# Kernel tuning notes

Hardware: AMD Instinct MI355X
Metric: run time of the kernel (lower is better)

The kernel has to match this reference:

```python
import jax, jax.numpy as jnp
import numpy as np

N_NODES = 50000
N_EDGES = 500000
N_REL = 50


def _linear(x, w, b):
    return x @ w.T + b


def _sage(x, src, dst, w_l, b_l, w_r, n_nodes):
    # PyG SAGEConv (mean aggr): out = lin_l(mean_{j in N(i)} x_j) + lin_r(x_i)
    msg = x[src]                                            # [E, F]
    s = jax.ops.segment_sum(msg, dst, num_segments=n_nodes)  # [N, F]
    cnt = jax.ops.segment_sum(jnp.ones((src.shape[0],), x.dtype), dst, num_segments=n_nodes)
    mean = s / jnp.clip(cnt, 1.0)[:, None]
    return mean @ w_l.T + b_l + x @ w_r.T


def setup_inputs() -> dict:
    key = jax.random.key(0)
    ks = jax.random.split(key, 24)

    def g(k, shape, fan_in):
        return jax.random.normal(k, shape, dtype=jnp.float32) * (1.0 / np.sqrt(fan_in))

    x = jax.random.normal(ks[0], (N_NODES, 16), dtype=jnp.float32)
    edge_index = jax.random.randint(ks[1], (2, N_EDGES), 0, N_NODES, dtype=jnp.int32)
    y = jax.random.randint(ks[2], (N_EDGES,), 0, N_REL, dtype=jnp.int32)

    return {
        "x": x, "edge_index": edge_index, "y": y,
        # SAGEConv 1: 16 -> 64
        "w1_l": g(ks[3], (64, 16), 16), "b1": jnp.zeros((64,), jnp.float32), "w1_r": g(ks[4], (64, 16), 16),
        # SAGEConv 2: 64 -> 128
        "w2_l": g(ks[5], (128, 64), 64), "b2": jnp.zeros((128,), jnp.float32), "w2_r": g(ks[6], (128, 64), 64),
        # object_fc: 256->128->64->32->16
        "of_w1": g(ks[7], (128, 256), 256), "of_b1": jnp.zeros((128,), jnp.float32),
        "of_w2": g(ks[8], (64, 128), 128), "of_b2": jnp.zeros((64,), jnp.float32),
        "of_w3": g(ks[9], (32, 64), 64), "of_b3": jnp.zeros((32,), jnp.float32),
        "of_w4": g(ks[10], (16, 32), 32), "of_b4": jnp.zeros((16,), jnp.float32),
        # relation_fc: 16->8->4->N_REL
        "rf_w1": g(ks[11], (8, 16), 16), "rf_b1": jnp.zeros((8,), jnp.float32),
        "rf_w2": g(ks[12], (4, 8), 8), "rf_b2": jnp.zeros((4,), jnp.float32),
        "rf_w3": g(ks[13], (N_REL, 4), 4), "rf_b3": jnp.zeros((N_REL,), jnp.float32),
    }


def reference(x, edge_index, y,
              w1_l, b1, w1_r, w2_l, b2, w2_r,
              of_w1, of_b1, of_w2, of_b2, of_w3, of_b3, of_w4, of_b4,
              rf_w1, rf_b1, rf_w2, rf_b2, rf_w3, rf_b3):
    src, dst = edge_index[0], edge_index[1]
    n = x.shape[0]

    h = jax.nn.relu(_sage(x, src, dst, w1_l, b1, w1_r, n))      # [N, 64]
    h = jax.nn.relu(_sage(h, src, dst, w2_l, b2, w2_r, n))      # [N, 128]

    # Batched version of the per-edge loop: gather endpoints, concat, MLP.
    feat = jnp.concatenate([h[src], h[dst]], axis=-1)           # [E, 256]
    o = jax.nn.relu(_linear(feat, of_w1, of_b1))   # dropout = identity (eval)
    o = jax.nn.relu(_linear(o, of_w2, of_b2))
    o = jax.nn.relu(_linear(o, of_w3, of_b3))
    o = _linear(o, of_w4, of_b4)                                # [E, 16]

    r = jax.nn.relu(_linear(o, rf_w1, rf_b1))
    r = jax.nn.relu(_linear(r, rf_w2, rf_b2))
    r = _linear(r, rf_w3, rf_b3)                                # [E, N_REL]
    return r, y
```

## Files before the change

### kernel.cpp

```cpp
#include <hip/hip_runtime.h>
#include <hip/hip_bf16.h>

#define N_NODES 50000
#define N_EDGES 500000
#define N_REL   50
#define NTILES  ((N_EDGES + 63) / 64)
#define PBLOCKS 512
#define NODE_TILES ((N_NODES + 63) / 64)

#define CNT_OFF 0
#define S1_OFF  (N_NODES)
#define S2_OFF  (S1_OFF + N_NODES*16)
#define ZERO_FLOATS (S2_OFF + N_NODES*64)
#define H1_OFF  ZERO_FLOATS
#define H2_OFF  (H1_OFF + N_NODES*64)

typedef short short8  __attribute__((ext_vector_type(8)));
typedef short short4v __attribute__((ext_vector_type(4)));
typedef float f32x4   __attribute__((ext_vector_type(4)));
typedef float f4      __attribute__((ext_vector_type(4)));

#define MFMA16(a,b,c) __builtin_amdgcn_mfma_f32_16x16x32_bf16((a),(b),(c),0,0,0)

__device__ __forceinline__ short f2bf(float x) {
    unsigned u = __float_as_uint(x);
    unsigned r = (u + 0x7fffu + ((u >> 16) & 1u)) >> 16;
    return (short)r;
}

__device__ __forceinline__ short8 load_wfrag(const float* __restrict__ W, int row, int K, int k) {
    const f4* p = (const f4*)(W + (size_t)row * K + k);
    f4 a = p[0], b = p[1];
    short8 r;
    r[0] = f2bf(a[0]); r[1] = f2bf(a[1]); r[2] = f2bf(a[2]); r[3] = f2bf(a[3]);
    r[4] = f2bf(b[0]); r[5] = f2bf(b[1]); r[6] = f2bf(b[2]); r[7] = f2bf(b[3]);
    return r;
}


__global__ __launch_bounds__(256) void k_scatter1(
    const float* __restrict__ x, const int* __restrict__ src,
    const int* __restrict__ dst, float* __restrict__ s1, float* __restrict__ cnt)
{
    int t = blockIdx.x * blockDim.x + threadIdx.x;
    if (t >= N_EDGES * 16) return;
    int e = t >> 4, f = t & 15;
    int s = src[e], d = dst[e];
    atomicAdd(&s1[d * 16 + f], x[s * 16 + f]);
    if (f == 0) atomicAdd(&cnt[d], 1.0f);
}

__global__ __launch_bounds__(256) void k_scatter2(
    const float* __restrict__ h1, const int* __restrict__ src,
    const int* __restrict__ dst, float* __restrict__ s2)
{
    long long t = (long long)blockIdx.x * blockDim.x + threadIdx.x;
    if (t >= (long long)N_EDGES * 64) return;
    int e = (int)(t >> 6), f = (int)(t & 63);
    atomicAdd(&s2[(long long)dst[e] * 64 + f], h1[(long long)src[e] * 64 + f]);
}

__global__ __launch_bounds__(256) void k_sage1_mfma(
    const float* __restrict__ x, const float* __restrict__ s1,
    const float* __restrict__ cnt,
    const float* __restrict__ w1_l, const float* __restrict__ b1,
    const float* __restrict__ w1_r, float* __restrict__ h1)
{
    __shared__ short feat[64 * 40];

    const int t    = threadIdx.x;
    const int w    = t >> 6;
    const int lane = t & 63;
    const int lr   = lane & 15;
    const int lg   = lane >> 4;
    const int base = blockIdx.x * 64;

    short8 w1f;
    if (lg < 2) w1f = load_wfrag(w1_l, w * 16 + lr, 16, lg * 8);
    else        w1f = load_wfrag(w1_r, w * 16 + lr, 16, (lg - 2) * 8);

    {
        int e  = t >> 2, q = t & 3;
        int ng = base + e;
        short8 v = (short8)0;
        if (ng < N_NODES) {
            if (q < 2) {
                float c = cnt[ng];
                c = c < 1.0f ? 1.0f : c;
                float inv = 1.0f / c;
                f4 a = *(const f4*)(s1 + (size_t)ng * 16 + q * 8);
                f4 b = *(const f4*)(s1 + (size_t)ng * 16 + q * 8 + 4);
#pragma unroll
                for (int j = 0; j < 4; ++j) { v[j] = f2bf(a[j] * inv); v[4 + j] = f2bf(b[j] * inv); }
            } else {
                f4 a = *(const f4*)(x + (size_t)ng * 16 + (q - 2) * 8);
                f4 b = *(const f4*)(x + (size_t)ng * 16 + (q - 2) * 8 + 4);
#pragma unroll
                for (int j = 0; j < 4; ++j) { v[j] = f2bf(a[j]); v[4 + j] = f2bf(b[j]); }
            }
        }
        *(short8*)&feat[e * 40 + q * 8] = v;
    }
    __syncthreads();

    f32x4 acc[4];
    f4 bia = *(const f4*)&b1[w * 16 + lg * 4];
#pragma unroll
    for (int nt = 0; nt < 4; ++nt) {
        acc[nt][0] = bia[0]; acc[nt][1] = bia[1]; acc[nt][2] = bia[2]; acc[nt][3] = bia[3];
    }
#pragma unroll
    for (int nt = 0; nt < 4; ++nt) {
        int e = nt * 16 + lr;
        short8 bf = *(const short8*)&feat[e * 40 + lg * 8];
        acc[nt] = MFMA16(w1f, bf, acc[nt]);
    }
#pragma unroll
    for (int nt = 0; nt < 4; ++nt) {
        int ng = base + nt * 16 + lr;
        if (ng < N_NODES) {
            f4 o;
#pragma unroll
            for (int r = 0; r < 4; ++r) { float v = acc[nt][r]; o[r] = v > 0.0f ? v : 0.0f; }
            *(f4*)&h1[(size_t)ng * 64 + w * 16 + lg * 4] = o;
        }
    }
}

__global__ __launch_bounds__(256) void k_sage2_mfma(
    const float* __restrict__ h1, const float* __restrict__ s2,
    const float* __restrict__ cnt,
    const float* __restrict__ w2_l, const float* __restrict__ b2,
    const float* __restrict__ w2_r, float* __restrict__ h2)
{
    __shared__ short feat[64 * 128];

    const int t    = threadIdx.x;
    const int w    = t >> 6;
    const int lane = t & 63;
    const int lr   = lane & 15;
    const int lg   = lane >> 4;
    const int base = blockIdx.x * 64;

    short8 wf[2][4];
#pragma unroll
    for (int mt = 0; mt < 2; ++mt)
#pragma unroll
        for (int kt = 0; kt < 4; ++kt) {
            int row = w * 32 + mt * 16 + lr;
            int k   = kt * 32 + lg * 8;
            wf[mt][kt] = (k < 64) ? load_wfrag(w2_r, row, 64, k)
                                  : load_wfrag(w2_l, row, 64, k - 64);
        }

    {
        int e  = t >> 2, q = t & 3;
        int ng = base + e;
        float inv = 1.0f;
        const float* srcp = nullptr;
        if (ng < N_NODES) {
            if (q < 2) {
                srcp = h1 + (size_t)ng * 64 + q * 32;
            } else {
                float c = cnt[ng];
                c = c < 1.0f ? 1.0f : c;
                inv = 1.0f / c;
                srcp = s2 + (size_t)ng * 64 + (q - 2) * 32;
            }
        }
#pragma unroll
        for (int j = 0; j < 4; ++j) {
            short8 v = (short8)0;
            if (srcp) {
                f4 a = *(const f4*)(srcp + j * 8);
                f4 b = *(const f4*)(srcp + j * 8 + 4);
#pragma unroll
                for (int q2 = 0; q2 < 4; ++q2) { v[q2] = f2bf(a[q2] * inv); v[4 + q2] = f2bf(b[q2] * inv); }
            }
            int cc   = q * 4 + j;
            int scol = (cc * 8) ^ ((e & 7) << 3);
            *(short8*)&feat[e * 128 + scol] = v;
        }
    }
    __syncthreads();

    f32x4 acc[2][4];
#pragma unroll
    for (int mt = 0; mt < 2; ++mt) {
        f4 bia = *(const f4*)&b2[w * 32 + mt * 16 + lg * 4];
#pragma unroll
        for (int nt = 0; nt < 4; ++nt) {
            acc[mt][nt][0] = bia[0]; acc[mt][nt][1] = bia[1];
            acc[mt][nt][2] = bia[2]; acc[mt][nt][3] = bia[3];
        }
    }
#pragma unroll
    for (int kt = 0; kt < 4; ++kt) {
        short8 bf[4];
#pragma unroll
        for (int nt = 0; nt < 4; ++nt) {
            int e = nt * 16 + lr;
            int k = kt * 32 + lg * 8;
            int scol = k ^ ((e & 7) << 3);
            bf[nt] = *(const short8*)&feat[e * 128 + scol];
        }
#pragma unroll
        for (int mt = 0; mt < 2; ++mt)
#pragma unroll
            for (int nt = 0; nt < 4; ++nt)
                acc[mt][nt] = MFMA16(wf[mt][kt], bf[nt], acc[mt][nt]);
    }
#pragma unroll
    for (int mt = 0; mt < 2; ++mt)
#pragma unroll
        for (int nt = 0; nt < 4; ++nt) {
            int ng = base + nt * 16 + lr;
            if (ng < N_NODES) {
                f4 o;
#pragma unroll
                for (int r = 0; r < 4; ++r) { float v = acc[mt][nt][r]; o[r] = v > 0.0f ? v : 0.0f; }
                *(f4*)&h2[(size_t)ng * 128 + w * 32 + mt * 16 + lg * 4] = o;
            }
        }
}

__global__ __launch_bounds__(256, 2) void k_edge_fused(
    const float* __restrict__ h2, const int* __restrict__ src,
    const int* __restrict__ dst, const int* __restrict__ y,
    const float* __restrict__ ow1, const float* __restrict__ ob1,
    const float* __restrict__ ow2, const float* __restrict__ ob2,
    const float* __restrict__ ow3, const float* __restrict__ ob3,
    const float* __restrict__ ow4, const float* __restrict__ ob4,
    const float* __restrict__ rw1, const float* __restrict__ rb1,
    const float* __restrict__ rw2, const float* __restrict__ rb2,
    const float* __restrict__ rw3, const float* __restrict__ rb3,
    float* __restrict__ out)
{
    __shared__ short feat[64 * 256];
    __shared__ short act1[64 * 128];
    __shared__ float act4[64 * 17];
    __shared__ float act6[64 * 4];
    __shared__ float sw[662];

    short* act2 = feat;
    short* act3 = feat + 64 * 64;

    const int t    = threadIdx.x;
    const int w    = t >> 6;
    const int lane = t & 63;
    const int lr   = lane & 15;
    const int lg   = lane >> 4;

    if (t < 128) sw[t]       = ob1[t];
    if (t < 64)  sw[128 + t] = ob2[t];
    if (t < 32)  sw[192 + t] = ob3[t];
    if (t < 16)  sw[224 + t] = ob4[t];
    if (t < 8)   sw[240 + t] = rb1[t];
    if (t < 4)   sw[248 + t] = rb2[t];
    if (t < 50)  sw[252 + t] = rb3[t];
    if (t < 128) sw[302 + t] = rw1[t];
    if (t < 32)  sw[430 + t] = rw2[t];
    if (t < 200) sw[462 + t] = rw3[t];

    short8 w1f[2][8];
#pragma unroll
    for (int mt = 0; mt < 2; ++mt)
#pragma unroll
        for (int kt = 0; kt < 8; ++kt)
            w1f[mt][kt] = load_wfrag(ow1, w * 32 + mt * 16 + lr, 256, kt * 32 + lg * 8);

    short8 w2f[4];
#pragma unroll
    for (int kt = 0; kt < 4; ++kt)
        w2f[kt] = load_wfrag(ow2, w * 16 + lr, 128, kt * 32 + lg * 8);

    short8 w3f[2][2];
#pragma unroll
    for (int mt = 0; mt < 2; ++mt)
#pragma unroll
        for (int kt = 0; kt < 2; ++kt)
            w3f[mt][kt] = load_wfrag(ow3, mt * 16 + lr, 64, kt * 32 + lg * 8);

    short8 w4f = load_wfrag(ow4, lr, 32, lg * 8);

    for (int tile = blockIdx.x; tile < NTILES; tile += PBLOCKS) {
        const int base = tile * 64;

        {
            int e    = t >> 2;
            int half = (t >> 1) & 1;
            int eg   = base + e;
            const float* np = nullptr;
            if (eg < N_EDGES) {
                int node = half ? dst[eg] : src[eg];
                np = h2 + (size_t)node * 128 + (t & 1) * 64;
            }
#pragma unroll
            for (int j = 0; j < 8; ++j) {
                short8 v;
                if (np) {
                    f4 a = *(const f4*)(np + j * 8);
                    f4 b = *(const f4*)(np + j * 8 + 4);
                    v[0] = f2bf(a[0]); v[1] = f2bf(a[1]); v[2] = f2bf(a[2]); v[3] = f2bf(a[3]);
                    v[4] = f2bf(b[0]); v[5] = f2bf(b[1]); v[6] = f2bf(b[2]); v[7] = f2bf(b[3]);
                } else {
                    v = (short8)0;
                }
                int cc   = half * 16 + (t & 1) * 8 + j;
                int scol = (cc * 8) ^ ((e & 7) << 3);
                *(short8*)&feat[e * 256 + scol] = v;
            }
        }
        __syncthreads();

        {
            f32x4 acc[2][4];
#pragma unroll
            for (int mt = 0; mt < 2; ++mt) {
                f32x4 bia;
#pragma unroll
                for (int r = 0; r < 4; ++r) bia[r] = sw[w * 32 + mt * 16 + lg * 4 + r];
#pragma unroll
                for (int nt = 0; nt < 4; ++nt) acc[mt][nt] = bia;
            }
#pragma unroll
            for (int kt = 0; kt < 8; ++kt) {
                short8 bf[4];
#pragma unroll
                for (int nt = 0; nt < 4; ++nt) {
                    int e = nt * 16 + lr;
                    int k = kt * 32 + lg * 8;
                    int scol = k ^ ((e & 7) << 3);
                    bf[nt] = *(const short8*)&feat[e * 256 + scol];
                }
#pragma unroll
                for (int mt = 0; mt < 2; ++mt)
#pragma unroll
                    for (int nt = 0; nt < 4; ++nt)
                        acc[mt][nt] = MFMA16(w1f[mt][kt], bf[nt], acc[mt][nt]);
            }
#pragma unroll
            for (int mt = 0; mt < 2; ++mt)
#pragma unroll
                for (int nt = 0; nt < 4; ++nt) {
                    int e  = nt * 16 + lr;
                    int n0 = w * 32 + mt * 16 + lg * 4;
                    short4v s;
#pragma unroll
                    for (int r = 0; r < 4; ++r) {
                        float v = acc[mt][nt][r];
                        s[r] = f2bf(v > 0.0f ? v : 0.0f);
                    }
                    int scol = n0 ^ ((e & 7) << 3);
                    *(short4v*)&act1[e * 128 + scol] = s;
                }
        }
        __syncthreads();

        {
            f32x4 acc[4];
            f32x4 bia;
#pragma unroll
            for (int r = 0; r < 4; ++r) bia[r] = sw[128 + w * 16 + lg * 4 + r];
#pragma unroll
            for (int nt = 0; nt < 4; ++nt) acc[nt] = bia;
#pragma unroll
            for (int kt = 0; kt < 4; ++kt) {
#pragma unroll
                for (int nt = 0; nt < 4; ++nt) {
                    int e = nt * 16 + lr;
                    int k = kt * 32 + lg * 8;
                    int scol = k ^ ((e & 7) << 3);
                    short8 bf = *(const short8*)&act1[e * 128 + scol];
                    acc[nt] = MFMA16(w2f[kt], bf, acc[nt]);
                }
            }
#pragma unroll
            for (int nt = 0; nt < 4; ++nt) {
                int e  = nt * 16 + lr;
                int n0 = w * 16 + lg * 4;
                short4v s;
#pragma unroll
                for (int r = 0; r < 4; ++r) {
                    float v = acc[nt][r];
                    s[r] = f2bf(v > 0.0f ? v : 0.0f);
                }
                int scol = n0 ^ ((e & 7) << 3);
                *(short4v*)&act2[e * 64 + scol] = s;
            }
        }
        __syncthreads();

        {
            const int e3 = w * 16 + lr;
            f32x4 acc[2];
#pragma unroll
            for (int mt = 0; mt < 2; ++mt) {
#pragma unroll
                for (int r = 0; r < 4; ++r) acc[mt][r] = sw[192 + mt * 16 + lg * 4 + r];
            }
#pragma unroll
            for (int kt = 0; kt < 2; ++kt) {
                int k = kt * 32 + lg * 8;
                int scol = k ^ ((e3 & 7) << 3);
                short8 bf = *(const short8*)&act2[e3 * 64 + scol];
#pragma unroll
                for (int mt = 0; mt < 2; ++mt)
                    acc[mt] = MFMA16(w3f[mt][kt], bf, acc[mt]);
            }
#pragma unroll
            for (int mt = 0; mt < 2; ++mt) {
                short4v s;
#pragma unroll
                for (int r = 0; r < 4; ++r) {
                    float v = acc[mt][r];
                    s[r] = f2bf(v > 0.0f ? v : 0.0f);
                }
                *(short4v*)&act3[e3 * 32 + mt * 16 + lg * 4] = s;
            }

            short8 bf = *(const short8*)&act3[e3 * 32 + lg * 8];
            f32x4 a4;
#pragma unroll
            for (int r = 0; r < 4; ++r) a4[r] = sw[224 + lg * 4 + r];
            a4 = MFMA16(w4f, bf, a4);
#pragma unroll
            for (int r = 0; r < 4; ++r) act4[e3 * 17 + lg * 4 + r] = a4[r];
        }
        __syncthreads();

        if (t < 64) {
            float a16[16];
#pragma unroll
            for (int f = 0; f < 16; ++f) a16[f] = act4[t * 17 + f];
            float a8[8];
#pragma unroll
            for (int o = 0; o < 8; ++o) {
                float v = sw[240 + o];
#pragma unroll
                for (int f = 0; f < 16; ++f) v += a16[f] * sw[302 + o * 16 + f];
                a8[o] = v > 0.0f ? v : 0.0f;
            }
            float a4v[4];
#pragma unroll
            for (int o = 0; o < 4; ++o) {
                float v = sw[248 + o];
#pragma unroll
                for (int f = 0; f < 8; ++f) v += a8[f] * sw[430 + o * 8 + f];
                a4v[o] = v > 0.0f ? v : 0.0f;
            }
#pragma unroll
            for (int q = 0; q < 4; ++q) act6[t * 4 + q] = a4v[q];
            int eg = base + t;
            if (eg < N_EDGES) out[(size_t)N_EDGES * N_REL + eg] = (float)y[eg];
        }
        __syncthreads();

#pragma unroll
        for (int i = 0; i < 13; ++i) {
            int idx = t + i * 256;
            if (idx < 64 * N_REL) {
                int e  = idx / N_REL;
                int r  = idx - e * N_REL;
                int eg = base + e;
                if (eg < N_EDGES) {
                    float v = sw[252 + r];
#pragma unroll
                    for (int f = 0; f < 4; ++f) v += act6[e * 4 + f] * sw[462 + r * 4 + f];
                    out[(size_t)base * N_REL + idx] = v;
                }
            }
        }
        __syncthreads();
    }
}

extern "C" void kernel_launch(void* const* d_in, const int* in_sizes, int n_in,
                              void* d_out, int out_size, void* d_ws, size_t ws_size,
                              hipStream_t stream) {
    const float* x    = (const float*)d_in[0];
    const int*   ei   = (const int*)d_in[1];
    const int*   src  = ei;
    const int*   dst  = ei + N_EDGES;
    const int*   y    = (const int*)d_in[2];
    const float* w1_l = (const float*)d_in[3];
    const float* b1   = (const float*)d_in[4];
    const float* w1_r = (const float*)d_in[5];
    const float* w2_l = (const float*)d_in[6];
    const float* b2   = (const float*)d_in[7];
    const float* w2_r = (const float*)d_in[8];
    const float* ow1  = (const float*)d_in[9];
    const float* ob1  = (const float*)d_in[10];
    const float* ow2  = (const float*)d_in[11];
    const float* ob2  = (const float*)d_in[12];
    const float* ow3  = (const float*)d_in[13];
    const float* ob3  = (const float*)d_in[14];
    const float* ow4  = (const float*)d_in[15];
    const float* ob4  = (const float*)d_in[16];
    const float* rw1  = (const float*)d_in[17];
    const float* rb1  = (const float*)d_in[18];
    const float* rw2  = (const float*)d_in[19];
    const float* rb2  = (const float*)d_in[20];
    const float* rw3  = (const float*)d_in[21];
    const float* rb3  = (const float*)d_in[22];

    float* ws  = (float*)d_ws;
    float* cnt = ws + CNT_OFF;
    float* s1  = ws + S1_OFF;
    float* s2  = ws + S2_OFF;
    float* h1  = ws + H1_OFF;
    float* h2  = ws + H2_OFF;
    float* out = (float*)d_out;

    hipMemsetAsync(d_ws, 0, (size_t)ZERO_FLOATS * sizeof(float), stream);

    {
        int total = N_EDGES * 16;
        k_scatter1<<<(total + 255) / 256, 256, 0, stream>>>(x, src, dst, s1, cnt);
    }
    k_sage1_mfma<<<NODE_TILES, 256, 0, stream>>>(x, s1, cnt, w1_l, b1, w1_r, h1);
    {
        long long total = (long long)N_EDGES * 64;
        k_scatter2<<<(int)((total + 255) / 256), 256, 0, stream>>>(h1, src, dst, s2);
    }
    k_sage2_mfma<<<NODE_TILES, 256, 0, stream>>>(h1, s2, cnt, w2_l, b2, w2_r, h2);

    k_edge_fused<<<PBLOCKS, 256, 0, stream>>>(
        h2, src, dst, y,
        ow1, ob1, ow2, ob2, ow3, ob3, ow4, ob4,
        rw1, rb1, rw2, rb2, rw3, rb3, out);
}
```

Measured before the change: 479.8 us.

## Store hidden activations in bf16, DMA edge gathers to LDS, per-wave MLP tail

Writes h1 and h2 as bf16 instead of fp32, which halves the gather traffic in the second scatter and the edge kernel. The edge kernel now gathers endpoint features directly into LDS with global_load_lds in a swizzled layout. The small relation MLP tail becomes a per-wave computation using wave barriers instead of block-wide syncs, and its scratch reuses the act1 buffer. Grid size and the occupancy hint rise from 2 to 3 blocks per CU. The bf16 rounding of h1 before aggregation adds a small precision loss.

After: 806.8 us. +68.2%, slower.

```diff
diff --git a/kernel.cpp b/kernel.cpp
--- a/kernel.cpp
+++ b/kernel.cpp
@@ -5,7 +5,7 @@
 #define N_EDGES 500000
 #define N_REL   50
 #define NTILES  ((N_EDGES + 63) / 64)
-#define PBLOCKS 512
+#define PBLOCKS 768
 #define NODE_TILES ((N_NODES + 63) / 64)
 
 #define CNT_OFF 0
@@ -26,6 +26,9 @@
     unsigned u = __float_as_uint(x);
     unsigned r = (u + 0x7fffu + ((u >> 16) & 1u)) >> 16;
     return (short)r;
+}
+__device__ __forceinline__ float bf2f(short s) {
+    return __uint_as_float(((unsigned)(unsigned short)s) << 16);
 }
 
 __device__ __forceinline__ short8 load_wfrag(const float* __restrict__ W, int row, int K, int k) {
@@ -35,6 +38,12 @@
     r[0] = f2bf(a[0]); r[1] = f2bf(a[1]); r[2] = f2bf(a[2]); r[3] = f2bf(a[3]);
     r[4] = f2bf(b[0]); r[5] = f2bf(b[1]); r[6] = f2bf(b[2]); r[7] = f2bf(b[3]);
     return r;
+}
+
+__device__ __forceinline__ void gload_lds16(const void* g, void* l) {
+    __builtin_amdgcn_global_load_lds(
+        (const __attribute__((address_space(1))) void*)g,
+        (__attribute__((address_space(3))) void*)l, 16, 0, 0);
 }
 
 
@@ -51,20 +60,24 @@
 }
 
 __global__ __launch_bounds__(256) void k_scatter2(
-    const float* __restrict__ h1, const int* __restrict__ src,
+    const short* __restrict__ h1b, const int* __restrict__ src,
     const int* __restrict__ dst, float* __restrict__ s2)
 {
-    long long t = (long long)blockIdx.x * blockDim.x + threadIdx.x;
-    if (t >= (long long)N_EDGES * 64) return;
-    int e = (int)(t >> 6), f = (int)(t & 63);
-    atomicAdd(&s2[(long long)dst[e] * 64 + f], h1[(long long)src[e] * 64 + f]);
+    int t = blockIdx.x * blockDim.x + threadIdx.x;
+    if (t >= N_EDGES * 16) return;
+    int e = t >> 4, q = t & 15;
+    int s = src[e], d = dst[e];
+    short4v v = *(const short4v*)&h1b[(size_t)s * 64 + q * 4];
+    float* p = &s2[(size_t)d * 64 + q * 4];
+#pragma unroll
+    for (int j = 0; j < 4; ++j) atomicAdd(p + j, bf2f(v[j]));
 }
 
 __global__ __launch_bounds__(256) void k_sage1_mfma(
     const float* __restrict__ x, const float* __restrict__ s1,
     const float* __restrict__ cnt,
     const float* __restrict__ w1_l, const float* __restrict__ b1,
-    const float* __restrict__ w1_r, float* __restrict__ h1)
+    const float* __restrict__ w1_r, short* __restrict__ h1b)
 {
     __shared__ short feat[64 * 40];
 
@@ -119,19 +132,19 @@
     for (int nt = 0; nt < 4; ++nt) {
         int ng = base + nt * 16 + lr;
         if (ng < N_NODES) {
-            f4 o;
-#pragma unroll
-            for (int r = 0; r < 4; ++r) { float v = acc[nt][r]; o[r] = v > 0.0f ? v : 0.0f; }
-            *(f4*)&h1[(size_t)ng * 64 + w * 16 + lg * 4] = o;
+            short4v o;
+#pragma unroll
+            for (int r = 0; r < 4; ++r) { float v = acc[nt][r]; o[r] = f2bf(v > 0.0f ? v : 0.0f); }
+            *(short4v*)&h1b[(size_t)ng * 64 + w * 16 + lg * 4] = o;
         }
     }
 }
 
 __global__ __launch_bounds__(256) void k_sage2_mfma(
-    const float* __restrict__ h1, const float* __restrict__ s2,
+    const short* __restrict__ h1b, const float* __restrict__ s2,
     const float* __restrict__ cnt,
     const float* __restrict__ w2_l, const float* __restrict__ b2,
-    const float* __restrict__ w2_r, float* __restrict__ h2)
+    const float* __restrict__ w2_r, short* __restrict__ h2b)
 {
     __shared__ short feat[64 * 128];
 
@@ -156,30 +169,37 @@
     {
         int e  = t >> 2, q = t & 3;
         int ng = base + e;
-        float inv = 1.0f;
-        const float* srcp = nullptr;
-        if (ng < N_NODES) {
-            if (q < 2) {
-                srcp = h1 + (size_t)ng * 64 + q * 32;
-            } else {
+        if (q < 2) {
+            const short* hp = (ng < N_NODES) ? (h1b + (size_t)ng * 64 + q * 32) : nullptr;
+#pragma unroll
+            for (int j = 0; j < 4; ++j) {
+                short8 v = hp ? *(const short8*)(hp + j * 8) : (short8)0;
+                int cc   = q * 4 + j;
+                int scol = (cc * 8) ^ ((e & 7) << 3);
+                *(short8*)&feat[e * 128 + scol] = v;
+            }
+        } else {
+            float inv = 1.0f;
+            const float* srcp = nullptr;
+            if (ng < N_NODES) {
                 float c = cnt[ng];
                 c = c < 1.0f ? 1.0f : c;
                 inv = 1.0f / c;
                 srcp = s2 + (size_t)ng * 64 + (q - 2) * 32;
             }
-        }
-#pragma unroll
-        for (int j = 0; j < 4; ++j) {
-            short8 v = (short8)0;
-            if (srcp) {
-                f4 a = *(const f4*)(srcp + j * 8);
-                f4 b = *(const f4*)(srcp + j * 8 + 4);
-#pragma unroll
-                for (int q2 = 0; q2 < 4; ++q2) { v[q2] = f2bf(a[q2] * inv); v[4 + q2] = f2bf(b[q2] * inv); }
-            }
-            int cc   = q * 4 + j;
-            int scol = (cc * 8) ^ ((e & 7) << 3);
-            *(short8*)&feat[e * 128 + scol] = v;
+#pragma unroll
+            for (int j = 0; j < 4; ++j) {
+                short8 v = (short8)0;
+                if (srcp) {
+                    f4 a = *(const f4*)(srcp + j * 8);
+                    f4 b = *(const f4*)(srcp + j * 8 + 4);
+#pragma unroll
+                    for (int q2 = 0; q2 < 4; ++q2) { v[q2] = f2bf(a[q2] * inv); v[4 + q2] = f2bf(b[q2] * inv); }
+                }
+                int cc   = q * 4 + j;
+                int scol = (cc * 8) ^ ((e & 7) << 3);
+                *(short8*)&feat[e * 128 + scol] = v;
+            }
         }
     }
     __syncthreads();
@@ -216,16 +236,16 @@
         for (int nt = 0; nt < 4; ++nt) {
             int ng = base + nt * 16 + lr;
             if (ng < N_NODES) {
-                f4 o;
-#pragma unroll
-                for (int r = 0; r < 4; ++r) { float v = acc[mt][nt][r]; o[r] = v > 0.0f ? v : 0.0f; }
-                *(f4*)&h2[(size_t)ng * 128 + w * 32 + mt * 16 + lg * 4] = o;
-            }
-        }
-}
-
-__global__ __launch_bounds__(256, 2) void k_edge_fused(
-    const float* __restrict__ h2, const int* __restrict__ src,
+                short4v o;
+#pragma unroll
+                for (int r = 0; r < 4; ++r) { float v = acc[mt][nt][r]; o[r] = f2bf(v > 0.0f ? v : 0.0f); }
+                *(short4v*)&h2b[(size_t)ng * 128 + w * 32 + mt * 16 + lg * 4] = o;
+            }
+        }
+}
+
+__global__ __launch_bounds__(256, 3) void k_edge_fused(
+    const short* __restrict__ h2b, const int* __restrict__ src,
     const int* __restrict__ dst, const int* __restrict__ y,
     const float* __restrict__ ow1, const float* __restrict__ ob1,
     const float* __restrict__ ow2, const float* __restrict__ ob2,
@@ -238,12 +258,11 @@
 {
     __shared__ short feat[64 * 256];
     __shared__ short act1[64 * 128];
-    __shared__ float act4[64 * 17];
-    __shared__ float act6[64 * 4];
     __shared__ float sw[662];
 
     short* act2 = feat;
     short* act3 = feat + 64 * 64;
+    float* tailf = (float*)act1;
 
     const int t    = threadIdx.x;
     const int w    = t >> 6;
@@ -286,30 +305,18 @@
     for (int tile = blockIdx.x; tile < NTILES; tile += PBLOCKS) {
         const int base = tile * 64;
 
-        {
-            int e    = t >> 2;
-            int half = (t >> 1) & 1;
-            int eg   = base + e;
-            const float* np = nullptr;
-            if (eg < N_EDGES) {
-                int node = half ? dst[eg] : src[eg];
-                np = h2 + (size_t)node * 128 + (t & 1) * 64;
-            }
-#pragma unroll
-            for (int j = 0; j < 8; ++j) {
-                short8 v;
-                if (np) {
-                    f4 a = *(const f4*)(np + j * 8);
-                    f4 b = *(const f4*)(np + j * 8 + 4);
-                    v[0] = f2bf(a[0]); v[1] = f2bf(a[1]); v[2] = f2bf(a[2]); v[3] = f2bf(a[3]);
-                    v[4] = f2bf(b[0]); v[5] = f2bf(b[1]); v[6] = f2bf(b[2]); v[7] = f2bf(b[3]);
-                } else {
-                    v = (short8)0;
-                }
-                int cc   = half * 16 + (t & 1) * 8 + j;
-                int scol = (cc * 8) ^ ((e & 7) << 3);
-                *(short8*)&feat[e * 256 + scol] = v;
-            }
+#pragma unroll
+        for (int i = 0; i < 8; ++i) {
+            int r0 = w * 16 + i * 2;
+            int e  = r0 + (lane >> 5);
+            int p  = lane & 31;
+            int u  = p ^ (e & 7);
+            int eg = base + e;
+            int ec = eg < N_EDGES ? eg : 0;
+            const int* ids = (u < 16) ? src : dst;
+            int node = ids[ec];
+            const short* g = h2b + (size_t)node * 128 + (u & 15) * 8;
+            gload_lds16(g, &feat[r0 * 256]);
         }
         __syncthreads();
 
@@ -393,12 +400,13 @@
 
         {
             const int e3 = w * 16 + lr;
+            float* T = tailf + w * 512;
+
             f32x4 acc[2];
 #pragma unroll
-            for (int mt = 0; mt < 2; ++mt) {
+            for (int mt = 0; mt < 2; ++mt)
 #pragma unroll
                 for (int r = 0; r < 4; ++r) acc[mt][r] = sw[192 + mt * 16 + lg * 4 + r];
-            }
 #pragma unroll
             for (int kt = 0; kt < 2; ++kt) {
                 int k = kt * 32 + lg * 8;
@@ -418,56 +426,60 @@
                 }
                 *(short4v*)&act3[e3 * 32 + mt * 16 + lg * 4] = s;
             }
-
-            short8 bf = *(const short8*)&act3[e3 * 32 + lg * 8];
-            f32x4 a4;
-#pragma unroll
-            for (int r = 0; r < 4; ++r) a4[r] = sw[224 + lg * 4 + r];
-            a4 = MFMA16(w4f, bf, a4);
-#pragma unroll
-            for (int r = 0; r < 4; ++r) act4[e3 * 17 + lg * 4 + r] = a4[r];
-        }
-        __syncthreads();
-
-        if (t < 64) {
-            float a16[16];
-#pragma unroll
-            for (int f = 0; f < 16; ++f) a16[f] = act4[t * 17 + f];
-            float a8[8];
-#pragma unroll
-            for (int o = 0; o < 8; ++o) {
-                float v = sw[240 + o];
-#pragma unroll
-                for (int f = 0; f < 16; ++f) v += a16[f] * sw[302 + o * 16 + f];
-                a8[o] = v > 0.0f ? v : 0.0f;
-            }
-            float a4v[4];
-#pragma unroll
-            for (int o = 0; o < 4; ++o) {
-                float v = sw[248 + o];
-#pragma unroll
-                for (int f = 0; f < 8; ++f) v += a8[f] * sw[430 + o * 8 + f];
-                a4v[o] = v > 0.0f ? v : 0.0f;
-            }
-#pragma unroll
-            for (int q = 0; q < 4; ++q) act6[t * 4 + q] = a4v[q];
-            int eg = base + t;
-            if (eg < N_EDGES) out[(size_t)N_EDGES * N_REL + eg] = (float)y[eg];
-        }
-        __syncthreads();
-
-#pragma unroll
-        for (int i = 0; i < 13; ++i) {
-            int idx = t + i * 256;
-            if (idx < 64 * N_REL) {
-                int e  = idx / N_REL;
-                int r  = idx - e * N_REL;
-                int eg = base + e;
-                if (eg < N_EDGES) {
-                    float v = sw[252 + r];
-#pragma unroll
-                    for (int f = 0; f < 4; ++f) v += act6[e * 4 + f] * sw[462 + r * 4 + f];
-                    out[(size_t)base * N_REL + idx] = v;
+            __builtin_amdgcn_wave_barrier();
+
+            {
+                short8 bf = *(const short8*)&act3[e3 * 32 + lg * 8];
+                f32x4 a4;
+#pragma unroll
+                for (int r = 0; r < 4; ++r) a4[r] = sw[224 + lg * 4 + r];
+                a4 = MFMA16(w4f, bf, a4);
+#pragma unroll
+                for (int r = 0; r < 4; ++r) T[lr * 17 + lg * 4 + r] = a4[r];
+            }
+            __builtin_amdgcn_wave_barrier();
+
+            {
+                float af[16];
+#pragma unroll
+                for (int f = 0; f < 16; ++f) af[f] = T[lr * 17 + f];
+#pragma unroll
+                for (int oo = 0; oo < 2; ++oo) {
+                    int o = lg * 2 + oo;
+                    float v = sw[240 + o];
+#pragma unroll
+                    for (int f = 0; f < 16; ++f) v += af[f] * sw[302 + o * 16 + f];
+                    T[272 + lr * 9 + o] = v > 0.0f ? v : 0.0f;
+                }
+            }
+            __builtin_amdgcn_wave_barrier();
+
+            {
+                float v = sw[248 + lg];
+#pragma unroll
+                for (int f = 0; f < 8; ++f) v += T[272 + lr * 9 + f] * sw[430 + lg * 8 + f];
+                T[416 + lr * 5 + lg] = v > 0.0f ? v : 0.0f;
+            }
+            __builtin_amdgcn_wave_barrier();
+
+            if (lane < 16) {
+                int eg = base + w * 16 + lane;
+                if (eg < N_EDGES) out[(size_t)N_EDGES * N_REL + eg] = (float)y[eg];
+            }
+
+            size_t obase = (size_t)(base + w * 16) * N_REL;
+#pragma unroll
+            for (int k2 = 0; k2 < 13; ++k2) {
+                int idx = k2 * 64 + lane;
+                if (idx < 16 * N_REL) {
+                    int el = idx / N_REL;
+                    int o  = idx - el * N_REL;
+                    if (base + w * 16 + el < N_EDGES) {
+                        float v = sw[252 + o];
+#pragma unroll
+                        for (int f = 0; f < 4; ++f) v += T[416 + el * 5 + f] * sw[462 + o * 4 + f];
+                        out[obase + idx] = v;
+                    }
                 }
             }
         }
@@ -508,8 +520,8 @@
     float* cnt = ws + CNT_OFF;
     float* s1  = ws + S1_OFF;
     float* s2  = ws + S2_OFF;
-    float* h1  = ws + H1_OFF;
-    float* h2  = ws + H2_OFF;
+    short* h1b = (short*)(ws + H1_OFF);
+    short* h2b = (short*)(ws + H2_OFF);
     float* out = (float*)d_out;
 
     hipMemsetAsync(d_ws, 0, (size_t)ZERO_FLOATS * sizeof(float), stream);
@@ -518,15 +530,15 @@
         int total = N_EDGES * 16;
         k_scatter1<<<(total + 255) / 256, 256, 0, stream>>>(x, src, dst, s1, cnt);
     }
-    k_sage1_mfma<<<NODE_TILES, 256, 0, stream>>>(x, s1, cnt, w1_l, b1, w1_r, h1);
+    k_sage1_mfma<<<NODE_TILES, 256, 0, stream>>>(x, s1, cnt, w1_l, b1, w1_r, h1b);
     {
-        long long total = (long long)N_EDGES * 64;
-        k_scatter2<<<(int)((total + 255) / 256), 256, 0, stream>>>(h1, src, dst, s2);
-    }
-    k_sage2_mfma<<<NODE_TILES, 256, 0, stream>>>(h1, s2, cnt, w2_l, b2, w2_r, h2);
+        int total = N_EDGES * 16;
+        k_scatter2<<<(total + 255) / 256, 256, 0, stream>>>(h1b, src, dst, s2);
+    }
+    k_sage2_mfma<<<NODE_TILES, 256, 0, stream>>>(h1b, s2, cnt, w2_l, b2, w2_r, h2b);
 
     k_edge_fused<<<PBLOCKS, 256, 0, stream>>>(
-        h2, src, dst, y,
+        h2b, src, dst, y,
         ow1, ob1, ow2, ob2, ow3, ob3, ow4, ob4,
         rw1, rb1, rw2, rb2, rw3, rb3, out);
 }
```
